# Optimization experiments

Measured on AMD Instinct MI355X. Metric: run time of the kernel, lower is better.

## Reference

```python
import jax, jax.numpy as jnp
import numpy as np

EMBED_DIM = 1024
NUM_HEADS = 16
HEAD_DIM = EMBED_DIM // NUM_HEADS


def setup_inputs() -> dict:
    key = jax.random.key(0)
    k_x, k_wqkv, k_bqkv, k_wo, k_bo = jax.random.split(key, 5)
    B, S, D = 4, 2048, EMBED_DIM
    x = jax.random.normal(k_x, (B, S, D), dtype=jnp.float32)
    # Dense(embed_dim*3): weight [D, 3D], bias [3D]
    w_qkv = jax.random.normal(k_wqkv, (D, 3 * D), dtype=jnp.float32) * (1.0 / np.sqrt(D))
    b_qkv = jnp.zeros((3 * D,), dtype=jnp.float32)
    # Dense(embed_dim): weight [D, D], bias [D]
    w_out = jax.random.normal(k_wo, (D, D), dtype=jnp.float32) * (1.0 / np.sqrt(D))
    b_out = jnp.zeros((D,), dtype=jnp.float32)
    return {"x": x, "w_qkv": w_qkv, "b_qkv": b_qkv, "w_out": w_out, "b_out": b_out}


def reference(x, w_qkv, b_qkv, w_out, b_out):
    B, S, D = x.shape
    H, Hd = NUM_HEADS, HEAD_DIM
    qkv = x @ w_qkv + b_qkv                      # [B, S, 3D]
    qkv = qkv.reshape(B, S, 3, H, Hd)
    qkv = jnp.transpose(qkv, (2, 0, 3, 1, 4))    # [3, B, H, S, Hd]
    q, k, v = qkv[0], qkv[1], qkv[2]
    scores = jnp.einsum('bhqd,bhkd->bhqk', q, k) / jnp.sqrt(jnp.float32(Hd))
    # causal mask: lower-triangular ones, applied as scores*mask + (1-mask)*(-1e9)
    mask = jnp.tril(jnp.ones((S, S), dtype=jnp.float32))[None, None]
    scores = scores * mask + (1.0 - mask) * -1e9
    attn = jax.nn.softmax(scores, axis=-1)       # [B, H, S, S]
    out = jnp.einsum('bhqk,bhkd->bhqd', attn, v) # [B, H, S, Hd]
    out = jnp.transpose(out, (0, 2, 1, 3)).reshape(B, S, D)
    return out @ w_out + b_out
```

## Files before the change

### kernel.cpp

```cpp
#include <hip/hip_runtime.h>
#include <hip/hip_bf16.h>

#define NUMH 16
#define HD   64
#define EMB  1024
#define SEQL 2048
#define BATCH 4

typedef __attribute__((ext_vector_type(8))) short bf16x8;
typedef __attribute__((ext_vector_type(4))) float f32x4;
typedef __attribute__((ext_vector_type(16))) float f32x16;

__device__ __forceinline__ unsigned short f2bf(float f) {
  union { float f; unsigned int u; } v; v.f = f;
  unsigned int u = v.u + 0x7fffu + ((v.u >> 16) & 1u);
  return (unsigned short)(u >> 16);
}

__device__ __forceinline__ unsigned int cvtpk(float lo, float hi) {
  unsigned int r;
  asm("v_cvt_pk_bf16_f32 %0, %1, %2" : "=v"(r) : "v"(lo), "v"(hi));
  return r;
}

#define GLOAD16(gp, lp)                                                        \
  __builtin_amdgcn_global_load_lds(                                            \
      (const __attribute__((address_space(1))) unsigned int*)(gp),             \
      (__attribute__((address_space(3))) unsigned int*)(lp), 16, 0, 0)

__global__ __launch_bounds__(256) void cvt_x(const float* __restrict__ src,
                                             unsigned short* __restrict__ dst) {
  const size_t i = ((size_t)blockIdx.x * 256 + threadIdx.x) * 8;
  float4 a = *(const float4*)(src + i);
  float4 b = *(const float4*)(src + i + 4);
  bf16x8 w;
  w[0]=(short)f2bf(a.x); w[1]=(short)f2bf(a.y); w[2]=(short)f2bf(a.z); w[3]=(short)f2bf(a.w);
  w[4]=(short)f2bf(b.x); w[5]=(short)f2bf(b.y); w[6]=(short)f2bf(b.z); w[7]=(short)f2bf(b.w);
  *(bf16x8*)(dst + i) = w;
}

__global__ __launch_bounds__(256) void tr_cvt(const float* __restrict__ src,
                                              unsigned short* __restrict__ dst,
                                              int R, int C) {
  __shared__ unsigned short t[32][34];
  const int tx = threadIdx.x & 31, ty = threadIdx.x >> 5;
  const int c0 = blockIdx.x * 32, r0 = blockIdx.y * 32;
#pragma unroll
  for (int i = 0; i < 4; ++i)
    t[ty + i * 8][tx] = f2bf(src[(size_t)(r0 + ty + i * 8) * C + c0 + tx]);
  __syncthreads();
#pragma unroll
  for (int i = 0; i < 4; ++i)
    dst[(size_t)(c0 + ty + i * 8) * R + r0 + tx] = t[tx][ty + i * 8];
}

__global__ __launch_bounds__(256, 3) void gemm_qkv(
    const unsigned short* __restrict__ A, const unsigned short* __restrict__ BT,
    const float* __restrict__ Bias,
    unsigned short* __restrict__ Qo, unsigned short* __restrict__ Ko,
    unsigned short* __restrict__ Vo) {
  __shared__ __align__(16) unsigned short As[128][32];
  __shared__ __align__(16) unsigned short Bs[128][32];
  const int tid = threadIdx.x, lane = tid & 63, wv = tid >> 6;
  const int l15 = lane & 15, lg = lane >> 4;
  const int wrow = (wv >> 1) * 64, wcol = (wv & 1) * 64;
  const int cpx = gridDim.x >> 3;
  const int wg = (blockIdx.x & 7) * cpx + (blockIdx.x >> 3);
  const int mbase = (wg / 24) * 128, nbase = (wg % 24) * 128;

  f32x4 acc[4][4];
#pragma unroll
  for (int i = 0; i < 4; ++i)
#pragma unroll
    for (int j = 0; j < 4; ++j) acc[i][j] = (f32x4){0.f, 0.f, 0.f, 0.f};

  const int c0 = wv * 64 + lane;
  const unsigned short* ga0 = A + (size_t)(mbase + (c0 >> 2)) * EMB + (c0 & 3) * 8;
  const unsigned short* ga1 = ga0 + (size_t)64 * EMB;
  const unsigned short* gb0 = BT + (size_t)(nbase + (c0 >> 2)) * EMB + (c0 & 3) * 8;
  const unsigned short* gb1 = gb0 + (size_t)64 * EMB;
  unsigned short* la0 = &As[0][0] + c0 * 8;
  unsigned short* lb0 = &Bs[0][0] + c0 * 8;

  for (int k0 = 0; k0 < EMB; k0 += 32) {
    __syncthreads();
    GLOAD16(ga0 + k0, la0);
    GLOAD16(ga1 + k0, la0 + 2048);
    GLOAD16(gb0 + k0, lb0);
    GLOAD16(gb1 + k0, lb0 + 2048);
    __syncthreads();
    bf16x8 af[4], bfr[4];
#pragma unroll
    for (int mf = 0; mf < 4; ++mf)
      af[mf] = *(const bf16x8*)&As[wrow + mf * 16 + l15][lg * 8];
#pragma unroll
    for (int nf = 0; nf < 4; ++nf)
      bfr[nf] = *(const bf16x8*)&Bs[wcol + nf * 16 + l15][lg * 8];
#pragma unroll
    for (int mf = 0; mf < 4; ++mf)
#pragma unroll
      for (int nf = 0; nf < 4; ++nf)
        acc[mf][nf] = __builtin_amdgcn_mfma_f32_16x16x32_bf16(af[mf], bfr[nf], acc[mf][nf], 0, 0, 0);
  }

#pragma unroll
  for (int nf = 0; nf < 4; ++nf) {
    const int n = nbase + wcol + nf * 16 + l15;
    const float bias = Bias[n];
    const int which = n >> 10, rem = n & 1023;
    const int h = rem >> 6, d = rem & 63;
    unsigned short* dst = (which == 0) ? Qo : (which == 1) ? Ko : Vo;
#pragma unroll
    for (int mf = 0; mf < 4; ++mf)
#pragma unroll
      for (int j = 0; j < 4; ++j) {
        const int m = mbase + wrow + mf * 16 + lg * 4 + j;
        const int bb = m >> 11, s = m & 2047;
        dst[((size_t)(bb * NUMH + h) * SEQL + s) * HD + d] = f2bf(acc[mf][nf][j] + bias);
      }
  }
}

__global__ __launch_bounds__(256, 3) void gemm_out(
    const unsigned short* __restrict__ A, const unsigned short* __restrict__ BT,
    const float* __restrict__ Bias, float* __restrict__ Out) {
  __shared__ __align__(16) unsigned short As[128][32];
  __shared__ __align__(16) unsigned short Bs[128][32];
  const int tid = threadIdx.x, lane = tid & 63, wv = tid >> 6;
  const int l15 = lane & 15, lg = lane >> 4;
  const int wrow = (wv >> 1) * 64, wcol = (wv & 1) * 64;
  const int cpx = gridDim.x >> 3;
  const int wg = (blockIdx.x & 7) * cpx + (blockIdx.x >> 3);
  const int mbase = (wg >> 3) * 128, nbase = (wg & 7) * 128;

  f32x4 acc[4][4];
#pragma unroll
  for (int i = 0; i < 4; ++i)
#pragma unroll
    for (int j = 0; j < 4; ++j) acc[i][j] = (f32x4){0.f, 0.f, 0.f, 0.f};

  const int c0 = wv * 64 + lane;
  const unsigned short* ga0 = A + (size_t)(mbase + (c0 >> 2)) * EMB + (c0 & 3) * 8;
  const unsigned short* ga1 = ga0 + (size_t)64 * EMB;
  const unsigned short* gb0 = BT + (size_t)(nbase + (c0 >> 2)) * EMB + (c0 & 3) * 8;
  const unsigned short* gb1 = gb0 + (size_t)64 * EMB;
  unsigned short* la0 = &As[0][0] + c0 * 8;
  unsigned short* lb0 = &Bs[0][0] + c0 * 8;

  for (int k0 = 0; k0 < EMB; k0 += 32) {
    __syncthreads();
    GLOAD16(ga0 + k0, la0);
    GLOAD16(ga1 + k0, la0 + 2048);
    GLOAD16(gb0 + k0, lb0);
    GLOAD16(gb1 + k0, lb0 + 2048);
    __syncthreads();
    bf16x8 af[4], bfr[4];
#pragma unroll
    for (int mf = 0; mf < 4; ++mf)
      af[mf] = *(const bf16x8*)&As[wrow + mf * 16 + l15][lg * 8];
#pragma unroll
    for (int nf = 0; nf < 4; ++nf)
      bfr[nf] = *(const bf16x8*)&Bs[wcol + nf * 16 + l15][lg * 8];
#pragma unroll
    for (int mf = 0; mf < 4; ++mf)
#pragma unroll
      for (int nf = 0; nf < 4; ++nf)
        acc[mf][nf] = __builtin_amdgcn_mfma_f32_16x16x32_bf16(af[mf], bfr[nf], acc[mf][nf], 0, 0, 0);
  }

#pragma unroll
  for (int nf = 0; nf < 4; ++nf) {
    const int n = nbase + wcol + nf * 16 + l15;
    const float bias = Bias[n];
#pragma unroll
    for (int mf = 0; mf < 4; ++mf)
#pragma unroll
      for (int j = 0; j < 4; ++j) {
        const int m = mbase + wrow + mf * 16 + lg * 4 + j;
        Out[(size_t)m * EMB + n] = acc[mf][nf][j] + bias;
      }
  }
}

__global__ __launch_bounds__(256, 3) void attn_fwd(
    const unsigned short* __restrict__ Q, const unsigned short* __restrict__ K,
    const unsigned short* __restrict__ V, unsigned short* __restrict__ O) {
  __shared__ __align__(16) unsigned short Ks[64][72];
  __shared__ __align__(16) unsigned short VT[64][72];
  const int tid = threadIdx.x, lane = tid & 63, wv = tid >> 6;
  const int l31 = lane & 31, hi = lane >> 5;
  const int d0 = blockIdx.x;
  const int qp = (d0 >> 3) & 7;
  const int bh = ((d0 & 7) << 3) | (d0 >> 6);
  const int b = bh >> 4, h = bh & 15;
  const size_t bho = (size_t)(b * NUMH + h) * SEQL * HD;
  const unsigned short* Qb = Q + bho;
  const unsigned short* Kb = K + bho;
  const unsigned short* Vb = V + bho;
  const float AS = 0.18033688011112042f;

  const int skrow = tid >> 2, skcol = (tid & 3) * 16;
  const int svrow = tid & 63, svd = (tid >> 6) * 16;

  for (int pass = 0; pass < 2; ++pass) {
    const int qt = pass ? (15 - qp) : qp;
    const int q0w = qt * 128 + wv * 32;
    const int qrow = q0w + l31;

    bf16x8 qf[4];
#pragma unroll
    for (int s = 0; s < 4; ++s)
      qf[s] = *(const bf16x8*)&Qb[(size_t)qrow * HD + s * 16 + hi * 8];

    f32x16 O0, O1;
#pragma unroll
    for (int i = 0; i < 16; ++i) { O0[i] = 0.f; O1[i] = 0.f; }
    float m_run = -1e30f, l_run = 0.f;

    const int nkt = 2 * qt + 2;
    for (int kt = 0; kt < nkt; ++kt) {
      const int ktb = kt * 64;
      __syncthreads();
      {
        const unsigned short* kp = &Kb[(size_t)(ktb + skrow) * HD + skcol];
        uint4 k0 = *(const uint4*)kp;
        uint4 k1 = *(const uint4*)(kp + 8);
        *(uint4*)&Ks[skrow][skcol] = k0;
        *(uint4*)&Ks[skrow][skcol + 8] = k1;
      }
      {
        const unsigned short* vp = &Vb[(size_t)(ktb + svrow) * HD + svd];
        union { uint4 u[2]; unsigned short s[16]; } vb;
        vb.u[0] = *(const uint4*)vp;
        vb.u[1] = *(const uint4*)(vp + 8);
#pragma unroll
        for (int i = 0; i < 16; ++i) VT[svd + i][svrow] = vb.s[i];
      }
      __syncthreads();

      if (ktb <= q0w + 31) {
        f32x16 S0, S1;
#pragma unroll
        for (int i = 0; i < 16; ++i) { S0[i] = 0.f; S1[i] = 0.f; }
#pragma unroll
        for (int s = 0; s < 4; ++s) {
          bf16x8 kf0 = *(const bf16x8*)&Ks[l31][s * 16 + hi * 8];
          bf16x8 kf1 = *(const bf16x8*)&Ks[32 + l31][s * 16 + hi * 8];
          S0 = __builtin_amdgcn_mfma_f32_32x32x16_bf16(kf0, qf[s], S0, 0, 0, 0);
          S1 = __builtin_amdgcn_mfma_f32_32x32x16_bf16(kf1, qf[s], S1, 0, 0, 0);
        }
        if (ktb + 63 > q0w) {
#pragma unroll
          for (int r = 0; r < 16; ++r) {
            const int kv0 = ktb + (r & 3) + 8 * (r >> 2) + 4 * hi;
            S0[r] = (kv0 > qrow) ? -1e30f : S0[r];
            S1[r] = (kv0 + 32 > qrow) ? -1e30f : S1[r];
          }
        }
        float t16[16];
#pragma unroll
        for (int i = 0; i < 16; ++i) t16[i] = fmaxf(S0[i], S1[i]);
#pragma unroll
        for (int i = 0; i < 8; ++i) t16[i] = fmaxf(t16[i], t16[i + 8]);
#pragma unroll
        for (int i = 0; i < 4; ++i) t16[i] = fmaxf(t16[i], t16[i + 4]);
        float mx = fmaxf(fmaxf(t16[0], t16[1]), fmaxf(t16[2], t16[3]));
        mx = fmaxf(mx, __shfl_xor(mx, 32));
        const float mn = fmaxf(m_run, mx);
        const float mk = mn * AS;
        const float sc = exp2f(__builtin_fmaf(m_run, AS, -mk));
        m_run = mn;
#pragma unroll
        for (int i = 0; i < 16; ++i) {
          S0[i] = exp2f(__builtin_fmaf(S0[i], AS, -mk));
          S1[i] = exp2f(__builtin_fmaf(S1[i], AS, -mk));
        }
        float a16[16];
#pragma unroll
        for (int i = 0; i < 16; ++i) a16[i] = S0[i] + S1[i];
#pragma unroll
        for (int i = 0; i < 8; ++i) a16[i] += a16[i + 8];
#pragma unroll
        for (int i = 0; i < 4; ++i) a16[i] += a16[i + 4];
        float rs = (a16[0] + a16[1]) + (a16[2] + a16[3]);
        rs += __shfl_xor(rs, 32);
        l_run = l_run * sc + rs;
#pragma unroll
        for (int i = 0; i < 16; ++i) { O0[i] *= sc; O1[i] *= sc; }

        unsigned int W[2][4][2], X[2][4][2];
#pragma unroll
        for (int g = 0; g < 4; ++g)
#pragma unroll
          for (int c = 0; c < 2; ++c) {
            W[0][g][c] = cvtpk(S0[4 * g + 2 * c], S0[4 * g + 2 * c + 1]);
            W[1][g][c] = cvtpk(S1[4 * g + 2 * c], S1[4 * g + 2 * c + 1]);
          }
#pragma unroll
        for (int t = 0; t < 2; ++t)
#pragma unroll
          for (int g = 0; g < 4; ++g)
#pragma unroll
            for (int c = 0; c < 2; ++c) X[t][g][c] = __shfl_xor(W[t][g][c], 32);

        bf16x8 Pf[4];
#pragma unroll
        for (int ks = 0; ks < 4; ++ks) {
          const int t = ks >> 1, k1 = ks & 1;
          union { unsigned int d[4]; bf16x8 v; } u;
          u.d[0] = hi ? X[t][2 * k1 + 1][0] : W[t][2 * k1][0];
          u.d[1] = hi ? X[t][2 * k1 + 1][1] : W[t][2 * k1][1];
          u.d[2] = hi ? W[t][2 * k1 + 1][0] : X[t][2 * k1][0];
          u.d[3] = hi ? W[t][2 * k1 + 1][1] : X[t][2 * k1][1];
          Pf[ks] = u.v;
        }
#pragma unroll
        for (int ks = 0; ks < 4; ++ks) {
          bf16x8 vf0 = *(const bf16x8*)&VT[l31][ks * 16 + hi * 8];
          bf16x8 vf1 = *(const bf16x8*)&VT[32 + l31][ks * 16 + hi * 8];
          O0 = __builtin_amdgcn_mfma_f32_32x32x16_bf16(vf0, Pf[ks], O0, 0, 0, 0);
          O1 = __builtin_amdgcn_mfma_f32_32x32x16_bf16(vf1, Pf[ks], O1, 0, 0, 0);
        }
      }
    }
    const float inv = 1.0f / l_run;
    unsigned short* Op = O + ((size_t)b * SEQL + qrow) * EMB + h * HD;
#pragma unroll
    for (int g = 0; g < 4; ++g) {
      unsigned int w00 = cvtpk(O0[4 * g] * inv, O0[4 * g + 1] * inv);
      unsigned int w01 = cvtpk(O0[4 * g + 2] * inv, O0[4 * g + 3] * inv);
      unsigned int w10 = cvtpk(O1[4 * g] * inv, O1[4 * g + 1] * inv);
      unsigned int w11 = cvtpk(O1[4 * g + 2] * inv, O1[4 * g + 3] * inv);
      const int dd = 8 * g + 4 * hi;
      *(uint2*)&Op[dd]      = uint2{w00, w01};
      *(uint2*)&Op[32 + dd] = uint2{w10, w11};
    }
  }
}

extern "C" void kernel_launch(void* const* d_in, const int* in_sizes, int n_in,
                              void* d_out, int out_size, void* d_ws, size_t ws_size,
                              hipStream_t stream) {
  const float* x     = (const float*)d_in[0];
  const float* w_qkv = (const float*)d_in[1];
  const float* b_qkv = (const float*)d_in[2];
  const float* w_out = (const float*)d_in[3];
  const float* b_out = (const float*)d_in[4];
  float* out = (float*)d_out;

  const size_t NE = (size_t)BATCH * NUMH * SEQL * HD;
  unsigned short* Qb = (unsigned short*)d_ws;
  unsigned short* Kb = Qb + NE;
  unsigned short* Vb = Kb + NE;
  unsigned short* AO = Vb + NE;
  unsigned short* xb = AO + NE;
  unsigned short* wqkvT = xb + NE;
  unsigned short* woutT = wqkvT + 3072 * 1024;

  cvt_x<<<dim3((unsigned)(NE / (256 * 8))), 256, 0, stream>>>(x, xb);
  tr_cvt<<<dim3(3072 / 32, 1024 / 32), 256, 0, stream>>>(w_qkv, wqkvT, 1024, 3072);
  tr_cvt<<<dim3(1024 / 32, 1024 / 32), 256, 0, stream>>>(w_out, woutT, 1024, 1024);

  gemm_qkv<<<dim3(1536), 256, 0, stream>>>(xb, wqkvT, b_qkv, Qb, Kb, Vb);
  attn_fwd<<<dim3(512), 256, 0, stream>>>(Qb, Kb, Vb, AO);
  gemm_out<<<dim3(512), 256, 0, stream>>>(AO, woutT, b_out, out);
}
```

Baseline: 273.9 us.

## Process both paired query tiles in one KV sweep with lazy rescaling

The attention kernel no longer runs two sequential passes over K/V, one per query tile. It processes tile qp and tile 15-qp together in a single loop, so each K/V tile is loaded and transposed into LDS once and shared by both. It also skips the online-softmax rescale unless the running max grows past a threshold, and uses permlane32_swap for the cross-half reductions. The cost is roughly doubled register pressure, so launch bounds drop from 3 to 2 blocks per SM.

```diff
diff --git a/kernel.cpp b/kernel.cpp
--- a/kernel.cpp
+++ b/kernel.cpp
@@ -21,6 +21,23 @@
   unsigned int r;
   asm("v_cvt_pk_bf16_f32 %0, %1, %2" : "=v"(r) : "v"(lo), "v"(hi));
   return r;
+}
+
+__device__ __forceinline__ float xhalf_max(float x) {
+#if __has_builtin(__builtin_amdgcn_permlane32_swap)
+  auto r = __builtin_amdgcn_permlane32_swap(__float_as_uint(x), __float_as_uint(x), false, false);
+  return fmaxf(__uint_as_float(r[0]), __uint_as_float(r[1]));
+#else
+  return fmaxf(x, __shfl_xor(x, 32));
+#endif
+}
+__device__ __forceinline__ float xhalf_sum(float x) {
+#if __has_builtin(__builtin_amdgcn_permlane32_swap)
+  auto r = __builtin_amdgcn_permlane32_swap(__float_as_uint(x), __float_as_uint(x), false, false);
+  return __uint_as_float(r[0]) + __uint_as_float(r[1]);
+#else
+  return x + __shfl_xor(x, 32);
+#endif
 }
 
 #define GLOAD16(gp, lp)                                                        \
@@ -182,7 +199,93 @@
   }
 }
 
-__global__ __launch_bounds__(256, 3) void attn_fwd(
+__device__ __forceinline__ void sm_pack(f32x16& S0, f32x16& S1, float& MR, float& LR,
+                                        f32x16& O0, f32x16& O1, bf16x8 Pf[4],
+                                        int ktb, int qrow, int q0w, int hi) {
+  const float AS = 0.18033688011112042f;
+  const float THRR = 44.36f;
+  if (ktb + 63 > q0w) {
+#pragma unroll
+    for (int r = 0; r < 16; ++r) {
+      const int kv0 = ktb + (r & 3) + 8 * (r >> 2) + 4 * hi;
+      S0[r] = (kv0 > qrow) ? -1e30f : S0[r];
+      S1[r] = (kv0 + 32 > qrow) ? -1e30f : S1[r];
+    }
+  }
+  float t[16];
+#pragma unroll
+  for (int i = 0; i < 16; ++i) t[i] = fmaxf(S0[i], S1[i]);
+#pragma unroll
+  for (int i = 0; i < 8; ++i) t[i] = fmaxf(t[i], t[i + 8]);
+#pragma unroll
+  for (int i = 0; i < 4; ++i) t[i] = fmaxf(t[i], t[i + 4]);
+  float mx = fmaxf(fmaxf(t[0], t[1]), fmaxf(t[2], t[3]));
+  mx = xhalf_max(mx);
+  if (!__all(mx - MR <= THRR)) {
+    const float mn = fmaxf(MR, mx);
+    const float sc = exp2f((MR - mn) * AS);
+    MR = mn;
+    LR *= sc;
+#pragma unroll
+    for (int i = 0; i < 16; ++i) { O0[i] *= sc; O1[i] *= sc; }
+  }
+  const float mk = MR * AS;
+#pragma unroll
+  for (int i = 0; i < 16; ++i) {
+    S0[i] = exp2f(__builtin_fmaf(S0[i], AS, -mk));
+    S1[i] = exp2f(__builtin_fmaf(S1[i], AS, -mk));
+  }
+  float a[16];
+#pragma unroll
+  for (int i = 0; i < 16; ++i) a[i] = S0[i] + S1[i];
+#pragma unroll
+  for (int i = 0; i < 8; ++i) a[i] += a[i + 8];
+#pragma unroll
+  for (int i = 0; i < 4; ++i) a[i] += a[i + 4];
+  LR += xhalf_sum((a[0] + a[1]) + (a[2] + a[3]));
+  unsigned int W[2][4][2], X[2][4][2];
+#pragma unroll
+  for (int g = 0; g < 4; ++g)
+#pragma unroll
+    for (int c = 0; c < 2; ++c) {
+      W[0][g][c] = cvtpk(S0[4 * g + 2 * c], S0[4 * g + 2 * c + 1]);
+      W[1][g][c] = cvtpk(S1[4 * g + 2 * c], S1[4 * g + 2 * c + 1]);
+    }
+#pragma unroll
+  for (int tt = 0; tt < 2; ++tt)
+#pragma unroll
+    for (int g = 0; g < 4; ++g)
+#pragma unroll
+      for (int c = 0; c < 2; ++c) X[tt][g][c] = __shfl_xor(W[tt][g][c], 32);
+
+#pragma unroll
+  for (int ks = 0; ks < 4; ++ks) {
+    const int tt = ks >> 1, k1 = ks & 1;
+    union { unsigned int d[4]; bf16x8 v; } u;
+    u.d[0] = hi ? X[tt][2 * k1 + 1][0] : W[tt][2 * k1][0];
+    u.d[1] = hi ? X[tt][2 * k1 + 1][1] : W[tt][2 * k1][1];
+    u.d[2] = hi ? W[tt][2 * k1 + 1][0] : X[tt][2 * k1][0];
+    u.d[3] = hi ? W[tt][2 * k1 + 1][1] : X[tt][2 * k1][1];
+    Pf[ks] = u.v;
+  }
+}
+
+__device__ __forceinline__ void write_o(unsigned short* Op, const f32x16& O0,
+                                        const f32x16& O1, float LR, int hi) {
+  const float inv = 1.0f / LR;
+#pragma unroll
+  for (int g = 0; g < 4; ++g) {
+    unsigned int w00 = cvtpk(O0[4 * g] * inv, O0[4 * g + 1] * inv);
+    unsigned int w01 = cvtpk(O0[4 * g + 2] * inv, O0[4 * g + 3] * inv);
+    unsigned int w10 = cvtpk(O1[4 * g] * inv, O1[4 * g + 1] * inv);
+    unsigned int w11 = cvtpk(O1[4 * g + 2] * inv, O1[4 * g + 3] * inv);
+    const int dd = 8 * g + 4 * hi;
+    *(uint2*)&Op[dd]      = uint2{w00, w01};
+    *(uint2*)&Op[32 + dd] = uint2{w10, w11};
+  }
+}
+
+__global__ __launch_bounds__(256, 2) void attn_fwd(
     const unsigned short* __restrict__ Q, const unsigned short* __restrict__ K,
     const unsigned short* __restrict__ V, unsigned short* __restrict__ O) {
   __shared__ __align__(16) unsigned short Ks[64][72];
@@ -197,145 +300,92 @@
   const unsigned short* Qb = Q + bho;
   const unsigned short* Kb = K + bho;
   const unsigned short* Vb = V + bho;
-  const float AS = 0.18033688011112042f;
+
+  const int qtA = qp, qtB = 15 - qp;
+  const int q0wA = qtA * 128 + wv * 32, q0wB = qtB * 128 + wv * 32;
+  const int qrowA = q0wA + l31, qrowB = q0wB + l31;
 
   const int skrow = tid >> 2, skcol = (tid & 3) * 16;
   const int svrow = tid & 63, svd = (tid >> 6) * 16;
 
-  for (int pass = 0; pass < 2; ++pass) {
-    const int qt = pass ? (15 - qp) : qp;
-    const int q0w = qt * 128 + wv * 32;
-    const int qrow = q0w + l31;
-
-    bf16x8 qf[4];
-#pragma unroll
-    for (int s = 0; s < 4; ++s)
-      qf[s] = *(const bf16x8*)&Qb[(size_t)qrow * HD + s * 16 + hi * 8];
-
-    f32x16 O0, O1;
-#pragma unroll
-    for (int i = 0; i < 16; ++i) { O0[i] = 0.f; O1[i] = 0.f; }
-    float m_run = -1e30f, l_run = 0.f;
-
-    const int nkt = 2 * qt + 2;
-    for (int kt = 0; kt < nkt; ++kt) {
-      const int ktb = kt * 64;
-      __syncthreads();
-      {
-        const unsigned short* kp = &Kb[(size_t)(ktb + skrow) * HD + skcol];
-        uint4 k0 = *(const uint4*)kp;
-        uint4 k1 = *(const uint4*)(kp + 8);
-        *(uint4*)&Ks[skrow][skcol] = k0;
-        *(uint4*)&Ks[skrow][skcol + 8] = k1;
-      }
-      {
-        const unsigned short* vp = &Vb[(size_t)(ktb + svrow) * HD + svd];
-        union { uint4 u[2]; unsigned short s[16]; } vb;
-        vb.u[0] = *(const uint4*)vp;
-        vb.u[1] = *(const uint4*)(vp + 8);
-#pragma unroll
-        for (int i = 0; i < 16; ++i) VT[svd + i][svrow] = vb.s[i];
-      }
-      __syncthreads();
-
-      if (ktb <= q0w + 31) {
-        f32x16 S0, S1;
-#pragma unroll
-        for (int i = 0; i < 16; ++i) { S0[i] = 0.f; S1[i] = 0.f; }
-#pragma unroll
-        for (int s = 0; s < 4; ++s) {
-          bf16x8 kf0 = *(const bf16x8*)&Ks[l31][s * 16 + hi * 8];
-          bf16x8 kf1 = *(const bf16x8*)&Ks[32 + l31][s * 16 + hi * 8];
-          S0 = __builtin_amdgcn_mfma_f32_32x32x16_bf16(kf0, qf[s], S0, 0, 0, 0);
-          S1 = __builtin_amdgcn_mfma_f32_32x32x16_bf16(kf1, qf[s], S1, 0, 0, 0);
-        }
-        if (ktb + 63 > q0w) {
-#pragma unroll
-          for (int r = 0; r < 16; ++r) {
-            const int kv0 = ktb + (r & 3) + 8 * (r >> 2) + 4 * hi;
-            S0[r] = (kv0 > qrow) ? -1e30f : S0[r];
-            S1[r] = (kv0 + 32 > qrow) ? -1e30f : S1[r];
-          }
-        }
-        float t16[16];
-#pragma unroll
-        for (int i = 0; i < 16; ++i) t16[i] = fmaxf(S0[i], S1[i]);
-#pragma unroll
-        for (int i = 0; i < 8; ++i) t16[i] = fmaxf(t16[i], t16[i + 8]);
-#pragma unroll
-        for (int i = 0; i < 4; ++i) t16[i] = fmaxf(t16[i], t16[i + 4]);
-        float mx = fmaxf(fmaxf(t16[0], t16[1]), fmaxf(t16[2], t16[3]));
-        mx = fmaxf(mx, __shfl_xor(mx, 32));
-        const float mn = fmaxf(m_run, mx);
-        const float mk = mn * AS;
-        const float sc = exp2f(__builtin_fmaf(m_run, AS, -mk));
-        m_run = mn;
-#pragma unroll
-        for (int i = 0; i < 16; ++i) {
-          S0[i] = exp2f(__builtin_fmaf(S0[i], AS, -mk));
-          S1[i] = exp2f(__builtin_fmaf(S1[i], AS, -mk));
-        }
-        float a16[16];
-#pragma unroll
-        for (int i = 0; i < 16; ++i) a16[i] = S0[i] + S1[i];
-#pragma unroll
-        for (int i = 0; i < 8; ++i) a16[i] += a16[i + 8];
-#pragma unroll
-        for (int i = 0; i < 4; ++i) a16[i] += a16[i + 4];
-        float rs = (a16[0] + a16[1]) + (a16[2] + a16[3]);
-        rs += __shfl_xor(rs, 32);
-        l_run = l_run * sc + rs;
-#pragma unroll
-        for (int i = 0; i < 16; ++i) { O0[i] *= sc; O1[i] *= sc; }
-
-        unsigned int W[2][4][2], X[2][4][2];
-#pragma unroll
-        for (int g = 0; g < 4; ++g)
-#pragma unroll
-          for (int c = 0; c < 2; ++c) {
-            W[0][g][c] = cvtpk(S0[4 * g + 2 * c], S0[4 * g + 2 * c + 1]);
-            W[1][g][c] = cvtpk(S1[4 * g + 2 * c], S1[4 * g + 2 * c + 1]);
-          }
-#pragma unroll
-        for (int t = 0; t < 2; ++t)
-#pragma unroll
-          for (int g = 0; g < 4; ++g)
-#pragma unroll
-            for (int c = 0; c < 2; ++c) X[t][g][c] = __shfl_xor(W[t][g][c], 32);
-
-        bf16x8 Pf[4];
-#pragma unroll
-        for (int ks = 0; ks < 4; ++ks) {
-          const int t = ks >> 1, k1 = ks & 1;
-          union { unsigned int d[4]; bf16x8 v; } u;
-          u.d[0] = hi ? X[t][2 * k1 + 1][0] : W[t][2 * k1][0];
-          u.d[1] = hi ? X[t][2 * k1 + 1][1] : W[t][2 * k1][1];
-          u.d[2] = hi ? W[t][2 * k1 + 1][0] : X[t][2 * k1][0];
-          u.d[3] = hi ? W[t][2 * k1 + 1][1] : X[t][2 * k1][1];
-          Pf[ks] = u.v;
-        }
-#pragma unroll
-        for (int ks = 0; ks < 4; ++ks) {
-          bf16x8 vf0 = *(const bf16x8*)&VT[l31][ks * 16 + hi * 8];
-          bf16x8 vf1 = *(const bf16x8*)&VT[32 + l31][ks * 16 + hi * 8];
-          O0 = __builtin_amdgcn_mfma_f32_32x32x16_bf16(vf0, Pf[ks], O0, 0, 0, 0);
-          O1 = __builtin_amdgcn_mfma_f32_32x32x16_bf16(vf1, Pf[ks], O1, 0, 0, 0);
-        }
-      }
-    }
-    const float inv = 1.0f / l_run;
-    unsigned short* Op = O + ((size_t)b * SEQL + qrow) * EMB + h * HD;
-#pragma unroll
-    for (int g = 0; g < 4; ++g) {
-      unsigned int w00 = cvtpk(O0[4 * g] * inv, O0[4 * g + 1] * inv);
-      unsigned int w01 = cvtpk(O0[4 * g + 2] * inv, O0[4 * g + 3] * inv);
-      unsigned int w10 = cvtpk(O1[4 * g] * inv, O1[4 * g + 1] * inv);
-      unsigned int w11 = cvtpk(O1[4 * g + 2] * inv, O1[4 * g + 3] * inv);
-      const int dd = 8 * g + 4 * hi;
-      *(uint2*)&Op[dd]      = uint2{w00, w01};
-      *(uint2*)&Op[32 + dd] = uint2{w10, w11};
-    }
-  }
+  bf16x8 qfA[4], qfB[4];
+#pragma unroll
+  for (int s = 0; s < 4; ++s) {
+    qfA[s] = *(const bf16x8*)&Qb[(size_t)qrowA * HD + s * 16 + hi * 8];
+    qfB[s] = *(const bf16x8*)&Qb[(size_t)qrowB * HD + s * 16 + hi * 8];
+  }
+
+  f32x16 OA0, OA1, OB0, OB1;
+#pragma unroll
+  for (int i = 0; i < 16; ++i) { OA0[i] = 0.f; OA1[i] = 0.f; OB0[i] = 0.f; OB1[i] = 0.f; }
+  float mA = -1e30f, lA = 0.f, mB = -1e30f, lB = 0.f;
+
+  const int nkt = 2 * qtB + 2;
+  for (int kt = 0; kt < nkt; ++kt) {
+    const int ktb = kt * 64;
+    __syncthreads();
+    {
+      const unsigned short* kp = &Kb[(size_t)(ktb + skrow) * HD + skcol];
+      *(uint4*)&Ks[skrow][skcol] = *(const uint4*)kp;
+      *(uint4*)&Ks[skrow][skcol + 8] = *(const uint4*)(kp + 8);
+    }
+    {
+      const unsigned short* vp = &Vb[(size_t)(ktb + svrow) * HD + svd];
+      union { uint4 u[2]; unsigned short s[16]; } vb;
+      vb.u[0] = *(const uint4*)vp;
+      vb.u[1] = *(const uint4*)(vp + 8);
+#pragma unroll
+      for (int i = 0; i < 16; ++i) VT[svd + i][svrow] = vb.s[i];
+    }
+    __syncthreads();
+
+    const bool aAct = (ktb <= q0wA + 31);
+    const bool bAct = (ktb <= q0wB + 31);
+
+    f32x16 SA0, SA1, SB0, SB1;
+    if (bAct) {
+#pragma unroll
+      for (int i = 0; i < 16; ++i) { SB0[i] = 0.f; SB1[i] = 0.f; }
+    }
+    if (aAct) {
+#pragma unroll
+      for (int i = 0; i < 16; ++i) { SA0[i] = 0.f; SA1[i] = 0.f; }
+    }
+#pragma unroll
+    for (int s = 0; s < 4; ++s) {
+      bf16x8 kf0 = *(const bf16x8*)&Ks[l31][s * 16 + hi * 8];
+      bf16x8 kf1 = *(const bf16x8*)&Ks[32 + l31][s * 16 + hi * 8];
+      if (bAct) {
+        SB0 = __builtin_amdgcn_mfma_f32_32x32x16_bf16(kf0, qfB[s], SB0, 0, 0, 0);
+        SB1 = __builtin_amdgcn_mfma_f32_32x32x16_bf16(kf1, qfB[s], SB1, 0, 0, 0);
+      }
+      if (aAct) {
+        SA0 = __builtin_amdgcn_mfma_f32_32x32x16_bf16(kf0, qfA[s], SA0, 0, 0, 0);
+        SA1 = __builtin_amdgcn_mfma_f32_32x32x16_bf16(kf1, qfA[s], SA1, 0, 0, 0);
+      }
+    }
+
+    bf16x8 PfA[4], PfB[4];
+    if (aAct) sm_pack(SA0, SA1, mA, lA, OA0, OA1, PfA, ktb, qrowA, q0wA, hi);
+    if (bAct) sm_pack(SB0, SB1, mB, lB, OB0, OB1, PfB, ktb, qrowB, q0wB, hi);
+
+#pragma unroll
+    for (int ks = 0; ks < 4; ++ks) {
+      bf16x8 vf0 = *(const bf16x8*)&VT[l31][ks * 16 + hi * 8];
+      bf16x8 vf1 = *(const bf16x8*)&VT[32 + l31][ks * 16 + hi * 8];
+      if (bAct) {
+        OB0 = __builtin_amdgcn_mfma_f32_32x32x16_bf16(vf0, PfB[ks], OB0, 0, 0, 0);
+        OB1 = __builtin_amdgcn_mfma_f32_32x32x16_bf16(vf1, PfB[ks], OB1, 0, 0, 0);
+      }
+      if (aAct) {
+        OA0 = __builtin_amdgcn_mfma_f32_32x32x16_bf16(vf0, PfA[ks], OA0, 0, 0, 0);
+        OA1 = __builtin_amdgcn_mfma_f32_32x32x16_bf16(vf1, PfA[ks], OA1, 0, 0, 0);
+      }
+    }
+  }
+
+  write_o(O + ((size_t)b * SEQL + qrowA) * EMB + h * HD, OA0, OA1, lA, hi);
+  write_o(O + ((size_t)b * SEQL + qrowB) * EMB + h * HD, OB0, OB1, lB, hi);
 }
 
 extern "C" void kernel_launch(void* const* d_in, const int* in_sizes, int n_in,
```

Result: slower. 297.7 us (+8.7%).
